# Performance work log

Measured on AMD Instinct MI355X. Metric: run time of the kernel, lower is better.

Reference implementation:

```python
import jax, jax.numpy as jnp
import numpy as np

H = 1024          # hidden_size
NH = 16           # num_attention_heads
HD = H // NH      # attention_head_size
EPS = 1e-12       # layer_norm_eps
NEG = jnp.finfo(jnp.float32).min


def setup_inputs() -> dict:
    key = jax.random.key(0)
    ks = jax.random.split(key, 12)
    B, S = 4, 2048
    sc = 1.0 / np.sqrt(H)
    return {
        "hidden_states": jax.random.normal(ks[0], (B, S, H), jnp.float32),
        "attention_mask": jnp.ones((B, S), jnp.float32),
        "Wq": jax.random.normal(ks[1], (H, H), jnp.float32) * sc,
        "bq": jnp.zeros((H,), jnp.float32),
        "Wk": jax.random.normal(ks[2], (H, H), jnp.float32) * sc,
        "bk": jnp.zeros((H,), jnp.float32),
        "Wv": jax.random.normal(ks[3], (H, H), jnp.float32) * sc,
        "bv": jnp.zeros((H,), jnp.float32),
        "Wo": jax.random.normal(ks[4], (H, H), jnp.float32) * sc,
        "bo": jnp.zeros((H,), jnp.float32),
        "ln_g": jnp.ones((H,), jnp.float32),
        "ln_b": jnp.zeros((H,), jnp.float32),
    }


def _split_heads(x):
    # (B, S, H) -> (B, NH, S, HD)
    B, S, _ = x.shape
    return x.reshape(B, S, NH, HD).transpose(0, 2, 1, 3)


def reference(hidden_states, attention_mask, Wq, bq, Wk, bk, Wv, bv, Wo, bo, ln_g, ln_b):
    q = _split_heads(hidden_states @ Wq + bq)
    k = _split_heads(hidden_states @ Wk + bk)
    v = _split_heads(hidden_states @ Wv + bv)

    # (B, NH, S, S)
    scores = jnp.einsum('bhqd,bhkd->bhqk', q, k) / jnp.sqrt(jnp.float32(HD))
    mask_add = (1.0 - attention_mask)[:, None, None, :] * NEG
    scores = scores + mask_add
    probs = jax.nn.softmax(scores, axis=-1)  # dropout is identity (eval / p=0)

    ctx = jnp.einsum('bhqk,bhkd->bhqd', probs, v)
    B, _, S, _ = ctx.shape
    ctx = ctx.transpose(0, 2, 1, 3).reshape(B, S, H)

    out = ctx @ Wo + bo
    x = out + hidden_states
    mu = jnp.mean(x, axis=-1, keepdims=True)
    var = jnp.var(x, axis=-1, keepdims=True)
    return (x - mu) * jax.lax.rsqrt(var + EPS) * ln_g + ln_b
```

## Files before the change

kernel.cpp:

```cpp
#include <hip/hip_runtime.h>
#include <stdint.h>

#define H_ 1024
#define NH_ 16
#define HD_ 64
#define B_ 4
#define S_ 2048
#define M_ (B_*S_)

typedef unsigned short u16;
typedef __attribute__((ext_vector_type(4))) unsigned short u16x4;
typedef __attribute__((ext_vector_type(8))) short bf16x8;
typedef __attribute__((ext_vector_type(4))) float f32x4;
typedef __attribute__((ext_vector_type(16))) float f32x16;
typedef __attribute__((ext_vector_type(4))) unsigned int u32x4;
typedef __attribute__((ext_vector_type(4))) int i32x4;

#define AS1 __attribute__((address_space(1)))
#define AS3 __attribute__((address_space(3)))

__device__ __forceinline__ void gload16(const void* g, void* l) {
  __builtin_amdgcn_global_load_lds((const AS1 void*)g, (AS3 void*)l, 16, 0, 0);
}

__device__ __forceinline__ u16 f2bf(float f) {
  union { float f; uint32_t u; } v; v.f = f;
  uint32_t u = v.u + 0x7FFFu + ((v.u >> 16) & 1u);
  return (u16)(u >> 16);
}

static __device__ __forceinline__ f32x4 mfma16(bf16x8 a, bf16x8 b, f32x4 c) {
  return __builtin_amdgcn_mfma_f32_16x16x32_bf16(a, b, c, 0, 0, 0);
}
static __device__ __forceinline__ f32x16 mfma32(bf16x8 a, bf16x8 b, f32x16 c) {
  return __builtin_amdgcn_mfma_f32_32x32x16_bf16(a, b, c, 0, 0, 0);
}

__device__ __forceinline__ int cvtpk(float lo, float hi) {
  int r;
  asm("v_cvt_pk_bf16_f32 %0, %1, %2" : "=v"(r) : "v"(lo), "v"(hi));
  return r;
}
__device__ __forceinline__ void plswap(int& a, int& b) {
  asm volatile("v_permlane32_swap_b32 %0, %1" : "+v"(a), "+v"(b));
}
#if __has_builtin(__builtin_amdgcn_exp2f)
#define EXP2F __builtin_amdgcn_exp2f
#else
#define EXP2F exp2f
#endif

__device__ __forceinline__ int xcd_swz(int bid, int nwg) {
  return (bid & 7) * (nwg >> 3) + (bid >> 3);
}


__global__ __launch_bounds__(256) void cvt_hs_kernel(const float* __restrict__ in, u16* __restrict__ out,
                                                     const float* __restrict__ mask, float* __restrict__ madd_g,
                                                     uint32_t* __restrict__ nzbits) {
  const int bid = blockIdx.x;
  if (bid < M_*H_/(256*8)) {
    int i = bid * 256 + threadIdx.x;
    const f32x4* p = (const f32x4*)in;
    f32x4 a = p[2*i], b = p[2*i+1];
    u32x4 o;
    o.x = (uint32_t)f2bf(a.x) | ((uint32_t)f2bf(a.y) << 16);
    o.y = (uint32_t)f2bf(a.z) | ((uint32_t)f2bf(a.w) << 16);
    o.z = (uint32_t)f2bf(b.x) | ((uint32_t)f2bf(b.y) << 16);
    o.w = (uint32_t)f2bf(b.z) | ((uint32_t)f2bf(b.w) << 16);
    ((u32x4*)out)[i] = o;
  } else {
    const int mb = bid - M_*H_/(256*8);
    int i = mb * 256 + threadIdx.x;
    f32x4 a = ((const f32x4*)mask)[2*i], b4 = ((const f32x4*)mask)[2*i+1];
    f32x4 ma, mb4;
    ma.x = (1.0f - a.x) * -3.0e38f;  ma.y = (1.0f - a.y) * -3.0e38f;
    ma.z = (1.0f - a.z) * -3.0e38f;  ma.w = (1.0f - a.w) * -3.0e38f;
    mb4.x = (1.0f - b4.x) * -3.0e38f; mb4.y = (1.0f - b4.y) * -3.0e38f;
    mb4.z = (1.0f - b4.z) * -3.0e38f; mb4.w = (1.0f - b4.w) * -3.0e38f;
    ((f32x4*)madd_g)[2*i] = ma;  ((f32x4*)madd_g)[2*i+1] = mb4;
    if (mb == 0) {
      const int t = threadIdx.x;
      if (t < B_) nzbits[t] = 0u;
      __syncthreads();
      if (t < B_*32) {
        int b = t >> 5, kt = t & 31;
        const float* mrow = mask + (size_t)b * S_ + kt*64;
        uint32_t nz = 0;
        for (int c = 0; c < 64; ++c) nz |= (mrow[c] != 1.0f) ? 1u : 0u;
        if (nz) atomicOr(&nzbits[b], 1u << kt);
      }
    }
  }
}

__global__ __launch_bounds__(256) void cvt_wT_kernel(const float* __restrict__ Wq, const float* __restrict__ Wk,
                                                     const float* __restrict__ Wv, const float* __restrict__ Wo,
                                                     u16* __restrict__ wt) {
  const int p = blockIdx.z;
  const float* W = (p == 0) ? Wq : (p == 1) ? Wk : (p == 2) ? Wv : Wo;
  __shared__ float tile[64][65];
  const int tr = blockIdx.y, tc = blockIdx.x, t = threadIdx.x;
#pragma unroll
  for (int it = 0; it < 16; ++it) {
    int idx = it * 256 + t, r = idx >> 6, c = idx & 63;
    tile[r][c] = W[(size_t)(tr*64 + r) * H_ + tc*64 + c];
  }
  __syncthreads();
  u16* outp = wt + (size_t)p * H_ * H_;
#pragma unroll
  for (int it = 0; it < 16; ++it) {
    int idx = it * 256 + t, r = idx >> 6, c = idx & 63;
    outp[(size_t)(tc*64 + r) * H_ + tr*64 + c] = f2bf(tile[c][r]);
  }
}


__device__ __forceinline__ void gemm_tile(const u16* __restrict__ A, const u16* __restrict__ Bt,
                                          int m0, int n0, u16* As, u16* Bs, f32x4 acc[4][4]) {
  const int tid = threadIdx.x;
  const int lane = tid & 63, wave = tid >> 6;
  const int wr = wave >> 1, wc = wave & 1;
  const int l15 = lane & 15, l4 = lane >> 4;
  const int r0 = tid >> 2, c0 = (tid & 3) * 8;
  const u16* Ap0 = A + (size_t)(m0 + r0) * H_ + c0;
  const u16* Ap1 = A + (size_t)(m0 + 64 + r0) * H_ + c0;
  const u16* Bp0 = Bt + (size_t)(n0 + r0) * H_ + c0;
  const u16* Bp1 = Bt + (size_t)(n0 + 64 + r0) * H_ + c0;
  u16* lA0 = As + (size_t)tid * 8;
  u16* lA1 = As + 2048 + (size_t)tid * 8;
  u16* lB0 = Bs + (size_t)tid * 8;
  u16* lB1 = Bs + 2048 + (size_t)tid * 8;
  for (int k0 = 0; k0 < H_; k0 += 32) {
    __syncthreads();
    gload16(Ap0 + k0, lA0);
    gload16(Ap1 + k0, lA1);
    gload16(Bp0 + k0, lB0);
    gload16(Bp1 + k0, lB1);
    __syncthreads();
    bf16x8 afr[4], bfr[4];
#pragma unroll
    for (int m = 0; m < 4; ++m) afr[m] = *(const bf16x8*)&As[(wr*64 + m*16 + l15) * 32 + l4*8];
#pragma unroll
    for (int n = 0; n < 4; ++n) bfr[n] = *(const bf16x8*)&Bs[(wc*64 + n*16 + l15) * 32 + l4*8];
#pragma unroll
    for (int m = 0; m < 4; ++m)
#pragma unroll
      for (int n = 0; n < 4; ++n)
        acc[m][n] = mfma16(afr[m], bfr[n], acc[m][n]);
  }
}

__global__ __launch_bounds__(256) void gemm_qkv_kernel(const u16* __restrict__ hs16, const u16* __restrict__ wt,
                                                       const float* __restrict__ bq, const float* __restrict__ bk,
                                                       const float* __restrict__ bv, u16* __restrict__ qkv16) {
  __shared__ __align__(16) u16 As[128*32], Bs[128*32];
  f32x4 acc[4][4] = {};
  const int lg = xcd_swz(blockIdx.x, 1536);
  const int m0 = (lg / 24) * 128, n0 = (lg % 24) * 128;
  gemm_tile(hs16, wt, m0, n0, As, Bs, acc);
  const int tid = threadIdx.x, lane = tid & 63, wave = tid >> 6;
  const int wr = wave >> 1, wc = wave & 1, l15 = lane & 15, l4 = lane >> 4;
  const int p = n0 >> 10;
  const float* bias = (p == 0) ? bq : (p == 1) ? bk : bv;
  const float qsc = (p == 0) ? 0.18033688f : 1.0f;
  u16* base = qkv16 + (size_t)p * ((size_t)B_*NH_*S_*HD_);
  if (p == 2) {
    const int b = m0 >> 11;
#pragma unroll
    for (int n = 0; n < 4; ++n) {
      int ncol = (n0 & 1023) + wc*64 + n*16 + l15;
      int h = ncol >> 6, d = ncol & 63;
      float bsv = bias[ncol];
#pragma unroll
      for (int m = 0; m < 4; ++m) {
        int s0 = (m0 & 2047) + wr*64 + m*16 + l4*4;
        u16x4 pk;
#pragma unroll
        for (int r = 0; r < 4; ++r) pk[r] = f2bf(acc[m][n][r] + bsv);
        *(u16x4*)(base + (((size_t)b*NH_ + h)*HD_ + d)*S_ + s0) = pk;
      }
    }
  } else {
#pragma unroll
    for (int n = 0; n < 4; ++n) {
      int ncol = (n0 & 1023) + wc*64 + n*16 + l15;
      int h = ncol >> 6, d = ncol & 63;
      float bsv = bias[ncol];
#pragma unroll
      for (int m = 0; m < 4; ++m) {
#pragma unroll
        for (int r = 0; r < 4; ++r) {
          int row = m0 + wr*64 + m*16 + l4*4 + r;
          int b = row >> 11, s = row & 2047;
          base[(((size_t)b*NH_ + h)*S_ + s)*HD_ + d] = f2bf((acc[m][n][r] + bsv) * qsc);
        }
      }
    }
  }
}

__global__ __launch_bounds__(256) void gemm_out_kernel(const u16* __restrict__ ctx16, const u16* __restrict__ wo,
                                                       const float* __restrict__ bo, const float* __restrict__ hs,
                                                       float* __restrict__ xout) {
  __shared__ __align__(16) u16 As[128*32], Bs[128*32];
  f32x4 acc[4][4] = {};
  const int lg = xcd_swz(blockIdx.x, 512);
  const int m0 = (lg / 8) * 128, n0 = (lg % 8) * 128;
  gemm_tile(ctx16, wo, m0, n0, As, Bs, acc);
  const int tid = threadIdx.x, lane = tid & 63, wave = tid >> 6;
  const int wr = wave >> 1, wc = wave & 1, l15 = lane & 15, l4 = lane >> 4;
#pragma unroll
  for (int n = 0; n < 4; ++n) {
    int col = n0 + wc*64 + n*16 + l15;
    float bsv = bo[col];
#pragma unroll
    for (int m = 0; m < 4; ++m) {
#pragma unroll
      for (int r = 0; r < 4; ++r) {
        int row = m0 + wr*64 + m*16 + l4*4 + r;
        size_t off = (size_t)row * H_ + col;
        xout[off] = acc[m][n][r] + bsv + hs[off];
      }
    }
  }
}


__global__ __launch_bounds__(256, 2) void attn_kernel(const u16* __restrict__ q_, const u16* __restrict__ k_,
                                                      const u16* __restrict__ vt_, const float* __restrict__ madd_g,
                                                      const uint32_t* __restrict__ nzbits,
                                                      u16* __restrict__ ctx16) {
  __shared__ __align__(16) u16 Ks[2][64*64], Vs[2][64*64];
  const int lgid = xcd_swz(blockIdx.x, 512);
  const int qb = lgid & 7, bh = lgid >> 3, h = bh & 15, b = bh >> 4;
  const int tid = threadIdx.x, lane = tid & 63, wave = tid >> 6;
  const int l31 = lane & 31, hi = lane >> 5;
  const size_t headoff = ((size_t)b * NH_ + h) * ((size_t)S_ * HD_);
  const u16* Q  = q_ + headoff;
  const u16* K  = k_ + headoff;
  const u16* Vt = vt_ + headoff;
  const uint32_t nzb = nzbits[b];
  const int qbase = qb*256 + wave*64;
  bf16x8 qfA[4], qfB[4];
#pragma unroll
  for (int st = 0; st < 4; ++st) {
    qfA[st] = *(const bf16x8*)(Q + (size_t)(qbase + l31) * HD_ + st*16 + hi*8);
    qfB[st] = *(const bf16x8*)(Q + (size_t)(qbase + 32 + l31) * HD_ + st*16 + hi*8);
  }
  union { i32x4 i; bf16x8 hv; } uo;
  uo.i = (i32x4){0x3F803F80, 0x3F803F80, 0x3F803F80, 0x3F803F80};
  const bf16x8 ones = uo.hv;
  f32x16 O00 = {}, O01 = {}, O10 = {}, O11 = {};
  f32x16 LA = {}, LB = {};
  const int srow = tid >> 3, sch = tid & 7;
  const int gch = sch ^ (srow & 7);
  const int swzA = l31 & 7;

#define STAGE(bb, kt) do { \
    const u16* Kt_ = K + (size_t)(kt) * 64 * HD_; \
    _Pragma("unroll") \
    for (int c = 0; c < 2; ++c) { \
      int row = c*32 + srow; \
      gload16(Kt_ + (size_t)row * HD_ + gch*8, &Ks[bb][c*2048 + (size_t)tid*8]); \
      gload16(Vt + (size_t)row * S_ + (kt)*64 + gch*8, &Vs[bb][c*2048 + (size_t)tid*8]); \
    } \
  } while (0)

  STAGE(0, 0);
  __syncthreads();

  for (int kt = 0; kt < 32; ++kt) {
    const int cur = kt & 1;
    const int nxt = (kt + 1) & 31;
    STAGE(cur ^ 1, nxt);
    asm volatile("s_waitcnt vmcnt(4)\n\ts_barrier" ::: "memory");
    f32x16 sA0 = {}, sA1 = {}, sB0 = {}, sB1 = {};
    __builtin_amdgcn_s_setprio(1);
#pragma unroll
    for (int st = 0; st < 4; ++st) {
      const int kch = ((2*st + hi) ^ swzA) * 8;
      bf16x8 kf0 = *(const bf16x8*)&Ks[cur][l31*64 + kch];
      bf16x8 kf1 = *(const bf16x8*)&Ks[cur][(32 + l31)*64 + kch];
      sA0 = mfma32(kf0, qfA[st], sA0);
      sA1 = mfma32(kf1, qfA[st], sA1);
      sB0 = mfma32(kf0, qfB[st], sB0);
      sB1 = mfma32(kf1, qfB[st], sB1);
    }
    __builtin_amdgcn_s_setprio(0);
    if ((nzb >> kt) & 1u) {
#pragma unroll
      for (int t = 0; t < 2; ++t) {
        f32x16& sa = t ? sA1 : sA0;
        f32x16& sb = t ? sB1 : sB0;
#pragma unroll
        for (int bq = 0; bq < 4; ++bq) {
          f32x4 md = *(const f32x4*)(madd_g + (size_t)b * S_ + kt*64 + t*32 + bq*8 + hi*4);
#pragma unroll
          for (int a = 0; a < 4; ++a) { sa[bq*4 + a] += md[a]; sb[bq*4 + a] += md[a]; }
        }
      }
    }
#pragma unroll
    for (int r = 0; r < 16; ++r) sA0[r] = EXP2F(sA0[r]);
#pragma unroll
    for (int r = 0; r < 16; ++r) sA1[r] = EXP2F(sA1[r]);
#pragma unroll
    for (int r = 0; r < 16; ++r) sB0[r] = EXP2F(sB0[r]);
#pragma unroll
    for (int r = 0; r < 16; ++r) sB1[r] = EXP2F(sB1[r]);
    __builtin_amdgcn_s_setprio(1);
#pragma unroll
    for (int ks = 0; ks < 4; ++ks) {
      const f32x16& sa = (ks < 2) ? sA0 : sA1;
      const f32x16& sb = (ks < 2) ? sB0 : sB1;
      const int p = ks & 1;
      int pa0 = cvtpk(sa[8*p+0], sa[8*p+1]);
      int pa1 = cvtpk(sa[8*p+2], sa[8*p+3]);
      int pa2 = cvtpk(sa[8*p+4], sa[8*p+5]);
      int pa3 = cvtpk(sa[8*p+6], sa[8*p+7]);
      plswap(pa0, pa2); plswap(pa1, pa3);
      union { i32x4 i; bf16x8 hv; } ua; ua.i = (i32x4){pa0, pa1, pa2, pa3};
      int pb0 = cvtpk(sb[8*p+0], sb[8*p+1]);
      int pb1 = cvtpk(sb[8*p+2], sb[8*p+3]);
      int pb2 = cvtpk(sb[8*p+4], sb[8*p+5]);
      int pb3 = cvtpk(sb[8*p+6], sb[8*p+7]);
      plswap(pb0, pb2); plswap(pb1, pb3);
      union { i32x4 i; bf16x8 hv; } ub; ub.i = (i32x4){pb0, pb1, pb2, pb3};
      const int vch = ((2*ks + hi) ^ swzA) * 8;
      bf16x8 vb0 = *(const bf16x8*)&Vs[cur][l31*64 + vch];
      bf16x8 vb1 = *(const bf16x8*)&Vs[cur][(32 + l31)*64 + vch];
      O00 = mfma32(ua.hv, vb0, O00);
      O01 = mfma32(ua.hv, vb1, O01);
      LA  = mfma32(ua.hv, ones,    LA);
      O10 = mfma32(ub.hv, vb0, O10);
      O11 = mfma32(ub.hv, vb1, O11);
      LB  = mfma32(ub.hv, ones,    LB);
    }
    __builtin_amdgcn_s_setprio(0);
    asm volatile("s_barrier" ::: "memory");
  }
  asm volatile("s_waitcnt vmcnt(0)" ::: "memory");
#pragma unroll
  for (int bq = 0; bq < 4; ++bq) {
#pragma unroll
    for (int a = 0; a < 4; ++a) {
      int ql = 8*bq + 4*hi + a, r = bq*4 + a;
      float iA = 1.0f / LA[r], iB = 1.0f / LB[r];
      int sA_ = qbase + ql;
      size_t ob0 = ((size_t)(b * S_ + sA_) * NH_ + h) * HD_;
      ctx16[ob0 + l31]      = f2bf(O00[r] * iA);
      ctx16[ob0 + 32 + l31] = f2bf(O01[r] * iA);
      int sB_ = qbase + 32 + ql;
      size_t ob1 = ((size_t)(b * S_ + sB_) * NH_ + h) * HD_;
      ctx16[ob1 + l31]      = f2bf(O10[r] * iB);
      ctx16[ob1 + 32 + l31] = f2bf(O11[r] * iB);
    }
  }
#undef STAGE
}


__global__ __launch_bounds__(256) void ln_kernel(float* __restrict__ x, const float* __restrict__ g,
                                                 const float* __restrict__ bb) {
  const int row = blockIdx.x, t = threadIdx.x;
  float* xr = x + (size_t)row * H_;
  f32x4 v = ((const f32x4*)xr)[t];
  float s = v.x + v.y + v.z + v.w;
  float s2 = v.x*v.x + v.y*v.y + v.z*v.z + v.w*v.w;
#pragma unroll
  for (int o = 1; o < 64; o <<= 1) { s += __shfl_xor(s, o, 64); s2 += __shfl_xor(s2, o, 64); }
  __shared__ float red[8];
  const int wave = t >> 6, lane = t & 63;
  if (lane == 0) { red[wave] = s; red[4 + wave] = s2; }
  __syncthreads();
  s = red[0] + red[1] + red[2] + red[3];
  s2 = red[4] + red[5] + red[6] + red[7];
  const float mu = s * (1.0f / H_);
  const float var = s2 * (1.0f / H_) - mu * mu;
  const float rs = rsqrtf(var + 1e-12f);
  f32x4 gg = ((const f32x4*)g)[t], bb4 = ((const f32x4*)bb)[t];
  f32x4 o;
  o.x = (v.x - mu) * rs * gg.x + bb4.x;
  o.y = (v.y - mu) * rs * gg.y + bb4.y;
  o.z = (v.z - mu) * rs * gg.z + bb4.z;
  o.w = (v.w - mu) * rs * gg.w + bb4.w;
  ((f32x4*)xr)[t] = o;
}


extern "C" void kernel_launch(void* const* d_in, const int* in_sizes, int n_in,
                              void* d_out, int out_size, void* d_ws, size_t ws_size,
                              hipStream_t stream) {
  (void)in_sizes; (void)n_in; (void)out_size; (void)ws_size;
  const float* hs   = (const float*)d_in[0];
  const float* mask = (const float*)d_in[1];
  const float* Wq = (const float*)d_in[2];
  const float* bq = (const float*)d_in[3];
  const float* Wk = (const float*)d_in[4];
  const float* bk = (const float*)d_in[5];
  const float* Wv = (const float*)d_in[6];
  const float* bv = (const float*)d_in[7];
  const float* Wo = (const float*)d_in[8];
  const float* bo = (const float*)d_in[9];
  const float* lg = (const float*)d_in[10];
  const float* lb = (const float*)d_in[11];
  float* out = (float*)d_out;

  uint8_t* w = (uint8_t*)d_ws;
  u16* hs16  = (u16*)w;
  u16* wt16  = (u16*)(w + ((size_t)16 << 20));
  u16* qkv16 = (u16*)(w + ((size_t)24 << 20));
  u16* ctx16 = (u16*)(w + ((size_t)72 << 20));
  float* madd_g = (float*)(w + ((size_t)88 << 20));
  uint32_t* nzbits = (uint32_t*)(w + ((size_t)88 << 20) + 32768);

  const size_t psz = (size_t)B_*NH_*S_*HD_;
  cvt_hs_kernel<<<dim3(M_*H_/(256*8) + 4), dim3(256), 0, stream>>>(hs, hs16, mask, madd_g, nzbits);
  cvt_wT_kernel<<<dim3(16, 16, 4), dim3(256), 0, stream>>>(Wq, Wk, Wv, Wo, wt16);
  gemm_qkv_kernel<<<dim3(1536), dim3(256), 0, stream>>>(hs16, wt16, bq, bk, bv, qkv16);
  attn_kernel<<<dim3(512), dim3(256), 0, stream>>>(qkv16, qkv16 + psz, qkv16 + 2*psz, madd_g, nzbits, ctx16);
  gemm_out_kernel<<<dim3(512), dim3(256), 0, stream>>>(ctx16, wt16 + (size_t)3*H_*H_, bo, hs, out);
  ln_kernel<<<dim3(M_), dim3(256), 0, stream>>>(out, lg, lb);
}
```

Before: 208.9 us.

## Double-buffer GEMM tiles with 128x256 blocks and 32x32 MFMA

Replaces the single-buffered 128x128 GEMM loop with a double-buffered 128x256 tile. The next K-slice is prefetched via global_load_lds while the current one computes, using a partial vmcnt wait and raw barriers. Inner products switch from 16x16x32 to 32x32x16 bf16 MFMA, and the epilogues are remapped to the new accumulator layout. This halves the grid sizes, which cuts sync stalls and improves operand reuse, at the cost of fewer blocks (256 for the output GEMM) and more LDS per block.

```diff
diff --git a/kernel.cpp b/kernel.cpp
--- a/kernel.cpp
+++ b/kernel.cpp
@@ -29,9 +29,6 @@
   return (u16)(u >> 16);
 }
 
-static __device__ __forceinline__ f32x4 mfma16(bf16x8 a, bf16x8 b, f32x4 c) {
-  return __builtin_amdgcn_mfma_f32_16x16x32_bf16(a, b, c, 0, 0, 0);
-}
 static __device__ __forceinline__ f32x16 mfma32(bf16x8 a, bf16x8 b, f32x16 c) {
   return __builtin_amdgcn_mfma_f32_32x32x16_bf16(a, b, c, 0, 0, 0);
 }
@@ -116,111 +113,129 @@
 }
 
 
-__device__ __forceinline__ void gemm_tile(const u16* __restrict__ A, const u16* __restrict__ Bt,
-                                          int m0, int n0, u16* As, u16* Bs, f32x4 acc[4][4]) {
+__device__ __forceinline__ void gstage(const u16* __restrict__ A, const u16* __restrict__ Bt,
+                                       int m0, int n0, int k0, u16* As, u16* Bs, int tid) {
+#pragma unroll
+  for (int i = 0; i < 2; ++i) {
+    int c = i*256 + tid;
+    gload16(A + (size_t)(m0 + (c >> 2)) * H_ + k0 + (c & 3)*8, As + (size_t)c*8);
+  }
+#pragma unroll
+  for (int i = 0; i < 4; ++i) {
+    int c = i*256 + tid;
+    gload16(Bt + (size_t)(n0 + (c >> 2)) * H_ + k0 + (c & 3)*8, Bs + (size_t)c*8);
+  }
+}
+
+__device__ __forceinline__ void gemm_tile256(const u16* __restrict__ A, const u16* __restrict__ Bt,
+                                             int m0, int n0, u16* As, u16* Bs, f32x16 acc[2][4]) {
   const int tid = threadIdx.x;
   const int lane = tid & 63, wave = tid >> 6;
   const int wr = wave >> 1, wc = wave & 1;
-  const int l15 = lane & 15, l4 = lane >> 4;
-  const int r0 = tid >> 2, c0 = (tid & 3) * 8;
-  const u16* Ap0 = A + (size_t)(m0 + r0) * H_ + c0;
-  const u16* Ap1 = A + (size_t)(m0 + 64 + r0) * H_ + c0;
-  const u16* Bp0 = Bt + (size_t)(n0 + r0) * H_ + c0;
-  const u16* Bp1 = Bt + (size_t)(n0 + 64 + r0) * H_ + c0;
-  u16* lA0 = As + (size_t)tid * 8;
-  u16* lA1 = As + 2048 + (size_t)tid * 8;
-  u16* lB0 = Bs + (size_t)tid * 8;
-  u16* lB1 = Bs + 2048 + (size_t)tid * 8;
-  for (int k0 = 0; k0 < H_; k0 += 32) {
-    __syncthreads();
-    gload16(Ap0 + k0, lA0);
-    gload16(Ap1 + k0, lA1);
-    gload16(Bp0 + k0, lB0);
-    gload16(Bp1 + k0, lB1);
-    __syncthreads();
-    bf16x8 afr[4], bfr[4];
-#pragma unroll
-    for (int m = 0; m < 4; ++m) afr[m] = *(const bf16x8*)&As[(wr*64 + m*16 + l15) * 32 + l4*8];
-#pragma unroll
-    for (int n = 0; n < 4; ++n) bfr[n] = *(const bf16x8*)&Bs[(wc*64 + n*16 + l15) * 32 + l4*8];
-#pragma unroll
-    for (int m = 0; m < 4; ++m)
-#pragma unroll
-      for (int n = 0; n < 4; ++n)
-        acc[m][n] = mfma16(afr[m], bfr[n], acc[m][n]);
-  }
-}
-
-__global__ __launch_bounds__(256) void gemm_qkv_kernel(const u16* __restrict__ hs16, const u16* __restrict__ wt,
-                                                       const float* __restrict__ bq, const float* __restrict__ bk,
-                                                       const float* __restrict__ bv, u16* __restrict__ qkv16) {
-  __shared__ __align__(16) u16 As[128*32], Bs[128*32];
-  f32x4 acc[4][4] = {};
-  const int lg = xcd_swz(blockIdx.x, 1536);
-  const int m0 = (lg / 24) * 128, n0 = (lg % 24) * 128;
-  gemm_tile(hs16, wt, m0, n0, As, Bs, acc);
+  const int l31 = lane & 31, hi = lane >> 5;
+  gstage(A, Bt, m0, n0, 0, As, Bs, tid);
+  __syncthreads();
+  for (int kt = 0; kt < 32; ++kt) {
+    const int cur = kt & 1;
+    const int nk = (kt + 1) & 31;
+    gstage(A, Bt, m0, n0, nk*32, As + (cur^1)*4096, Bs + (cur^1)*8192, tid);
+    asm volatile("s_waitcnt vmcnt(6)\n\ts_barrier" ::: "memory");
+    const u16* Ab = As + cur*4096;
+    const u16* Bb = Bs + cur*8192;
+#pragma unroll
+    for (int ks = 0; ks < 2; ++ks) {
+      bf16x8 af[2], bf[4];
+#pragma unroll
+      for (int ms = 0; ms < 2; ++ms)
+        af[ms] = *(const bf16x8*)&Ab[(wr*64 + ms*32 + l31)*32 + ks*16 + hi*8];
+#pragma unroll
+      for (int ns = 0; ns < 4; ++ns)
+        bf[ns] = *(const bf16x8*)&Bb[(wc*128 + ns*32 + l31)*32 + ks*16 + hi*8];
+#pragma unroll
+      for (int ms = 0; ms < 2; ++ms)
+#pragma unroll
+        for (int ns = 0; ns < 4; ++ns)
+          acc[ms][ns] = mfma32(af[ms], bf[ns], acc[ms][ns]);
+    }
+    asm volatile("s_barrier" ::: "memory");
+  }
+  asm volatile("s_waitcnt vmcnt(0)" ::: "memory");
+}
+
+__global__ __launch_bounds__(256, 2) void gemm_qkv_kernel(const u16* __restrict__ hs16, const u16* __restrict__ wt,
+                                                          const float* __restrict__ bq, const float* __restrict__ bk,
+                                                          const float* __restrict__ bv, u16* __restrict__ qkv16) {
+  __shared__ __align__(16) u16 As[2*128*32], Bs[2*256*32];
+  f32x16 acc[2][4] = {};
+  const int lg = xcd_swz(blockIdx.x, 768);
+  const int m0 = (lg / 12) * 128, n0 = (lg % 12) * 256;
+  gemm_tile256(hs16, wt, m0, n0, As, Bs, acc);
   const int tid = threadIdx.x, lane = tid & 63, wave = tid >> 6;
-  const int wr = wave >> 1, wc = wave & 1, l15 = lane & 15, l4 = lane >> 4;
+  const int wr = wave >> 1, wc = wave & 1, l31 = lane & 31, hi = lane >> 5;
   const int p = n0 >> 10;
+  const int ncb = (n0 & 1023) + wc*128;
   const float* bias = (p == 0) ? bq : (p == 1) ? bk : bv;
   const float qsc = (p == 0) ? 0.18033688f : 1.0f;
   u16* base = qkv16 + (size_t)p * ((size_t)B_*NH_*S_*HD_);
   if (p == 2) {
     const int b = m0 >> 11;
 #pragma unroll
-    for (int n = 0; n < 4; ++n) {
-      int ncol = (n0 & 1023) + wc*64 + n*16 + l15;
-      int h = ncol >> 6, d = ncol & 63;
-      float bsv = bias[ncol];
-#pragma unroll
-      for (int m = 0; m < 4; ++m) {
-        int s0 = (m0 & 2047) + wr*64 + m*16 + l4*4;
-        u16x4 pk;
-#pragma unroll
-        for (int r = 0; r < 4; ++r) pk[r] = f2bf(acc[m][n][r] + bsv);
-        *(u16x4*)(base + (((size_t)b*NH_ + h)*HD_ + d)*S_ + s0) = pk;
-      }
-    }
-  } else {
-#pragma unroll
-    for (int n = 0; n < 4; ++n) {
-      int ncol = (n0 & 1023) + wc*64 + n*16 + l15;
-      int h = ncol >> 6, d = ncol & 63;
-      float bsv = bias[ncol];
-#pragma unroll
-      for (int m = 0; m < 4; ++m) {
-#pragma unroll
-        for (int r = 0; r < 4; ++r) {
-          int row = m0 + wr*64 + m*16 + l4*4 + r;
-          int b = row >> 11, s = row & 2047;
-          base[(((size_t)b*NH_ + h)*S_ + s)*HD_ + d] = f2bf((acc[m][n][r] + bsv) * qsc);
+    for (int ns = 0; ns < 4; ++ns) {
+      int col = ncb + ns*32 + l31;
+      int h = col >> 6, d = col & 63;
+      float bsv = bias[col];
+#pragma unroll
+      for (int ms = 0; ms < 2; ++ms) {
+        int sb = (m0 & 2047) + wr*64 + ms*32 + 4*hi;
+#pragma unroll
+        for (int rq = 0; rq < 4; ++rq) {
+          u16x4 pk;
+#pragma unroll
+          for (int j = 0; j < 4; ++j) pk[j] = f2bf(acc[ms][ns][rq*4+j] + bsv);
+          *(u16x4*)(base + (((size_t)b*NH_ + h)*HD_ + d)*S_ + sb + 8*rq) = pk;
         }
       }
     }
-  }
-}
-
-__global__ __launch_bounds__(256) void gemm_out_kernel(const u16* __restrict__ ctx16, const u16* __restrict__ wo,
-                                                       const float* __restrict__ bo, const float* __restrict__ hs,
-                                                       float* __restrict__ xout) {
-  __shared__ __align__(16) u16 As[128*32], Bs[128*32];
-  f32x4 acc[4][4] = {};
-  const int lg = xcd_swz(blockIdx.x, 512);
-  const int m0 = (lg / 8) * 128, n0 = (lg % 8) * 128;
-  gemm_tile(ctx16, wo, m0, n0, As, Bs, acc);
+  } else {
+#pragma unroll
+    for (int ns = 0; ns < 4; ++ns) {
+      int col = ncb + ns*32 + l31;
+      int h = col >> 6, d = col & 63;
+      float bsv = bias[col];
+#pragma unroll
+      for (int ms = 0; ms < 2; ++ms) {
+#pragma unroll
+        for (int reg = 0; reg < 16; ++reg) {
+          int row = m0 + wr*64 + ms*32 + (reg&3) + 8*(reg>>2) + 4*hi;
+          int b = row >> 11, s = row & 2047;
+          base[(((size_t)b*NH_ + h)*S_ + s)*HD_ + d] = f2bf((acc[ms][ns][reg] + bsv) * qsc);
+        }
+      }
+    }
+  }
+}
+
+__global__ __launch_bounds__(256, 2) void gemm_out_kernel(const u16* __restrict__ ctx16, const u16* __restrict__ wo,
+                                                          const float* __restrict__ bo, const float* __restrict__ hs,
+                                                          float* __restrict__ xout) {
+  __shared__ __align__(16) u16 As[2*128*32], Bs[2*256*32];
+  f32x16 acc[2][4] = {};
+  const int lg = xcd_swz(blockIdx.x, 256);
+  const int m0 = (lg / 4) * 128, n0 = (lg % 4) * 256;
+  gemm_tile256(ctx16, wo, m0, n0, As, Bs, acc);
   const int tid = threadIdx.x, lane = tid & 63, wave = tid >> 6;
-  const int wr = wave >> 1, wc = wave & 1, l15 = lane & 15, l4 = lane >> 4;
-#pragma unroll
-  for (int n = 0; n < 4; ++n) {
-    int col = n0 + wc*64 + n*16 + l15;
+  const int wr = wave >> 1, wc = wave & 1, l31 = lane & 31, hi = lane >> 5;
+#pragma unroll
+  for (int ns = 0; ns < 4; ++ns) {
+    int col = n0 + wc*128 + ns*32 + l31;
     float bsv = bo[col];
 #pragma unroll
-    for (int m = 0; m < 4; ++m) {
-#pragma unroll
-      for (int r = 0; r < 4; ++r) {
-        int row = m0 + wr*64 + m*16 + l4*4 + r;
+    for (int ms = 0; ms < 2; ++ms) {
+#pragma unroll
+      for (int reg = 0; reg < 16; ++reg) {
+        int row = m0 + wr*64 + ms*32 + (reg&3) + 8*(reg>>2) + 4*hi;
         size_t off = (size_t)row * H_ + col;
-        xout[off] = acc[m][n][r] + bsv + hs[off];
+        xout[off] = acc[ms][ns][reg] + bsv + hs[off];
       }
     }
   }
@@ -418,8 +433,8 @@
   const size_t psz = (size_t)B_*NH_*S_*HD_;
   cvt_hs_kernel<<<dim3(M_*H_/(256*8) + 4), dim3(256), 0, stream>>>(hs, hs16, mask, madd_g, nzbits);
   cvt_wT_kernel<<<dim3(16, 16, 4), dim3(256), 0, stream>>>(Wq, Wk, Wv, Wo, wt16);
-  gemm_qkv_kernel<<<dim3(1536), dim3(256), 0, stream>>>(hs16, wt16, bq, bk, bv, qkv16);
+  gemm_qkv_kernel<<<dim3(768), dim3(256), 0, stream>>>(hs16, wt16, bq, bk, bv, qkv16);
   attn_kernel<<<dim3(512), dim3(256), 0, stream>>>(qkv16, qkv16 + psz, qkv16 + 2*psz, madd_g, nzbits, ctx16);
-  gemm_out_kernel<<<dim3(512), dim3(256), 0, stream>>>(ctx16, wt16 + (size_t)3*H_*H_, bo, hs, out);
+  gemm_out_kernel<<<dim3(256), dim3(256), 0, stream>>>(ctx16, wt16 + (size_t)3*H_*H_, bo, hs, out);
   ln_kernel<<<dim3(M_), dim3(256), 0, stream>>>(out, lg, lb);
 }
```

Result: slower. 232.3 us (+11.2%).

## Double-buffer GEMM LDS tiles and merge preprocessing kernels into one launch

Applied to the files above, without the earlier changes.

The shared GEMM tile loop now uses two LDS buffers. The next K-slice is prefetched with global_load_lds while MFMAs run on the current slice, using a vmcnt wait plus barrier in place of two full syncthreads per step. The hidden-state conversion, mask preparation and weight transpose kernels are merged into a single launch to remove one kernel launch. LDS use per GEMM block doubles, which may lower occupancy, and the last iteration issues a redundant wrapped prefetch.

```diff
diff --git a/kernel.cpp b/kernel.cpp
--- a/kernel.cpp
+++ b/kernel.cpp
@@ -55,12 +55,16 @@
 }
 
 
-__global__ __launch_bounds__(256) void cvt_hs_kernel(const float* __restrict__ in, u16* __restrict__ out,
-                                                     const float* __restrict__ mask, float* __restrict__ madd_g,
-                                                     uint32_t* __restrict__ nzbits) {
-  const int bid = blockIdx.x;
-  if (bid < M_*H_/(256*8)) {
-    int i = bid * 256 + threadIdx.x;
+__global__ __launch_bounds__(256) void prep_kernel(const float* __restrict__ in, u16* __restrict__ out,
+                                                   const float* __restrict__ mask, float* __restrict__ madd_g,
+                                                   uint32_t* __restrict__ nzbits,
+                                                   const float* __restrict__ Wq, const float* __restrict__ Wk,
+                                                   const float* __restrict__ Wv, const float* __restrict__ Wo,
+                                                   u16* __restrict__ wt) {
+  __shared__ float tile[64][65];
+  const int bid = blockIdx.x, t = threadIdx.x;
+  if (bid < 4096) {
+    int i = bid * 256 + t;
     const f32x4* p = (const f32x4*)in;
     f32x4 a = p[2*i], b = p[2*i+1];
     u32x4 o;
@@ -69,9 +73,9 @@
     o.z = (uint32_t)f2bf(b.x) | ((uint32_t)f2bf(b.y) << 16);
     o.w = (uint32_t)f2bf(b.z) | ((uint32_t)f2bf(b.w) << 16);
     ((u32x4*)out)[i] = o;
-  } else {
-    const int mb = bid - M_*H_/(256*8);
-    int i = mb * 256 + threadIdx.x;
+  } else if (bid < 4100) {
+    const int mb = bid - 4096;
+    int i = mb * 256 + t;
     f32x4 a = ((const f32x4*)mask)[2*i], b4 = ((const f32x4*)mask)[2*i+1];
     f32x4 ma, mb4;
     ma.x = (1.0f - a.x) * -3.0e38f;  ma.y = (1.0f - a.y) * -3.0e38f;
@@ -80,7 +84,6 @@
     mb4.z = (1.0f - b4.z) * -3.0e38f; mb4.w = (1.0f - b4.w) * -3.0e38f;
     ((f32x4*)madd_g)[2*i] = ma;  ((f32x4*)madd_g)[2*i+1] = mb4;
     if (mb == 0) {
-      const int t = threadIdx.x;
       if (t < B_) nzbits[t] = 0u;
       __syncthreads();
       if (t < B_*32) {
@@ -91,27 +94,22 @@
         if (nz) atomicOr(&nzbits[b], 1u << kt);
       }
     }
-  }
-}
-
-__global__ __launch_bounds__(256) void cvt_wT_kernel(const float* __restrict__ Wq, const float* __restrict__ Wk,
-                                                     const float* __restrict__ Wv, const float* __restrict__ Wo,
-                                                     u16* __restrict__ wt) {
-  const int p = blockIdx.z;
-  const float* W = (p == 0) ? Wq : (p == 1) ? Wk : (p == 2) ? Wv : Wo;
-  __shared__ float tile[64][65];
-  const int tr = blockIdx.y, tc = blockIdx.x, t = threadIdx.x;
-#pragma unroll
-  for (int it = 0; it < 16; ++it) {
-    int idx = it * 256 + t, r = idx >> 6, c = idx & 63;
-    tile[r][c] = W[(size_t)(tr*64 + r) * H_ + tc*64 + c];
-  }
-  __syncthreads();
-  u16* outp = wt + (size_t)p * H_ * H_;
-#pragma unroll
-  for (int it = 0; it < 16; ++it) {
-    int idx = it * 256 + t, r = idx >> 6, c = idx & 63;
-    outp[(size_t)(tc*64 + r) * H_ + tr*64 + c] = f2bf(tile[c][r]);
+  } else {
+    const int w = bid - 4100;
+    const int p = w >> 8, ti = w & 255, tr = ti >> 4, tc = ti & 15;
+    const float* W = (p == 0) ? Wq : (p == 1) ? Wk : (p == 2) ? Wv : Wo;
+#pragma unroll
+    for (int it = 0; it < 16; ++it) {
+      int idx = it * 256 + t, r = idx >> 6, c = idx & 63;
+      tile[r][c] = W[(size_t)(tr*64 + r) * H_ + tc*64 + c];
+    }
+    __syncthreads();
+    u16* outp = wt + (size_t)p * H_ * H_;
+#pragma unroll
+    for (int it = 0; it < 16; ++it) {
+      int idx = it * 256 + t, r = idx >> 6, c = idx & 63;
+      outp[(size_t)(tc*64 + r) * H_ + tr*64 + c] = f2bf(tile[c][r]);
+    }
   }
 }
 
@@ -127,34 +125,40 @@
   const u16* Ap1 = A + (size_t)(m0 + 64 + r0) * H_ + c0;
   const u16* Bp0 = Bt + (size_t)(n0 + r0) * H_ + c0;
   const u16* Bp1 = Bt + (size_t)(n0 + 64 + r0) * H_ + c0;
-  u16* lA0 = As + (size_t)tid * 8;
-  u16* lA1 = As + 2048 + (size_t)tid * 8;
-  u16* lB0 = Bs + (size_t)tid * 8;
-  u16* lB1 = Bs + 2048 + (size_t)tid * 8;
-  for (int k0 = 0; k0 < H_; k0 += 32) {
-    __syncthreads();
-    gload16(Ap0 + k0, lA0);
-    gload16(Ap1 + k0, lA1);
-    gload16(Bp0 + k0, lB0);
-    gload16(Bp1 + k0, lB1);
-    __syncthreads();
+#define GSTAGE(bb, k0) do { \
+    gload16(Ap0 + (k0), As + (bb)*4096 + (size_t)tid * 8); \
+    gload16(Ap1 + (k0), As + (bb)*4096 + 2048 + (size_t)tid * 8); \
+    gload16(Bp0 + (k0), Bs + (bb)*4096 + (size_t)tid * 8); \
+    gload16(Bp1 + (k0), Bs + (bb)*4096 + 2048 + (size_t)tid * 8); \
+  } while (0)
+  GSTAGE(0, 0);
+  for (int kt = 0; kt < 32; ++kt) {
+    const int cur = kt & 1;
+    const int nk = ((kt + 1) & 31) * 32;
+    GSTAGE(cur ^ 1, nk);
+    asm volatile("s_waitcnt vmcnt(4)\n\ts_barrier" ::: "memory");
+    const u16* Ab = As + cur*4096;
+    const u16* Bb = Bs + cur*4096;
     bf16x8 afr[4], bfr[4];
 #pragma unroll
-    for (int m = 0; m < 4; ++m) afr[m] = *(const bf16x8*)&As[(wr*64 + m*16 + l15) * 32 + l4*8];
-#pragma unroll
-    for (int n = 0; n < 4; ++n) bfr[n] = *(const bf16x8*)&Bs[(wc*64 + n*16 + l15) * 32 + l4*8];
+    for (int m = 0; m < 4; ++m) afr[m] = *(const bf16x8*)&Ab[(wr*64 + m*16 + l15) * 32 + l4*8];
+#pragma unroll
+    for (int n = 0; n < 4; ++n) bfr[n] = *(const bf16x8*)&Bb[(wc*64 + n*16 + l15) * 32 + l4*8];
 #pragma unroll
     for (int m = 0; m < 4; ++m)
 #pragma unroll
       for (int n = 0; n < 4; ++n)
         acc[m][n] = mfma16(afr[m], bfr[n], acc[m][n]);
-  }
+    asm volatile("s_barrier" ::: "memory");
+  }
+  asm volatile("s_waitcnt vmcnt(0)" ::: "memory");
+#undef GSTAGE
 }
 
 __global__ __launch_bounds__(256) void gemm_qkv_kernel(const u16* __restrict__ hs16, const u16* __restrict__ wt,
                                                        const float* __restrict__ bq, const float* __restrict__ bk,
                                                        const float* __restrict__ bv, u16* __restrict__ qkv16) {
-  __shared__ __align__(16) u16 As[128*32], Bs[128*32];
+  __shared__ __align__(16) u16 As[2*128*32], Bs[2*128*32];
   f32x4 acc[4][4] = {};
   const int lg = xcd_swz(blockIdx.x, 1536);
   const int m0 = (lg / 24) * 128, n0 = (lg % 24) * 128;
@@ -203,7 +207,7 @@
 __global__ __launch_bounds__(256) void gemm_out_kernel(const u16* __restrict__ ctx16, const u16* __restrict__ wo,
                                                        const float* __restrict__ bo, const float* __restrict__ hs,
                                                        float* __restrict__ xout) {
-  __shared__ __align__(16) u16 As[128*32], Bs[128*32];
+  __shared__ __align__(16) u16 As[2*128*32], Bs[2*128*32];
   f32x4 acc[4][4] = {};
   const int lg = xcd_swz(blockIdx.x, 512);
   const int m0 = (lg / 8) * 128, n0 = (lg % 8) * 128;
@@ -416,8 +420,8 @@
   uint32_t* nzbits = (uint32_t*)(w + ((size_t)88 << 20) + 32768);
 
   const size_t psz = (size_t)B_*NH_*S_*HD_;
-  cvt_hs_kernel<<<dim3(M_*H_/(256*8) + 4), dim3(256), 0, stream>>>(hs, hs16, mask, madd_g, nzbits);
-  cvt_wT_kernel<<<dim3(16, 16, 4), dim3(256), 0, stream>>>(Wq, Wk, Wv, Wo, wt16);
+  prep_kernel<<<dim3(5124), dim3(256), 0, stream>>>(hs, hs16, mask, madd_g, nzbits,
+                                                    Wq, Wk, Wv, Wo, wt16);
   gemm_qkv_kernel<<<dim3(1536), dim3(256), 0, stream>>>(hs16, wt16, bq, bk, bv, qkv16);
   attn_kernel<<<dim3(512), dim3(256), 0, stream>>>(qkv16, qkv16 + psz, qkv16 + 2*psz, madd_g, nzbits, ctx16);
   gemm_out_kernel<<<dim3(512), dim3(256), 0, stream>>>(ctx16, wt16 + (size_t)3*H_*H_, bo, hs, out);
```

Result: faster. 203.2 us (-2.7%).
